# Performance work log

Hardware: AMD Instinct MI355X
Metric: run time of the kernel (lower is better)

The kernel has to match this reference:

```python
import jax, jax.numpy as jnp
import numpy as np

T, B, V, E, NN, ON = 200, 64, 256, 512, 1024, 1024
INIT_P = 3.0


def _lstm_cell(x, h, c, W, b, nn):
    # x: [B, din], h/c: [B, nn], W: [din+nn, 4*nn]
    s = jnp.concatenate([x, h], axis=-1) @ W + b
    sigm_arg, tanh_arg = s[..., : 3 * nn], s[..., 3 * nn :]
    g = jax.nn.sigmoid(sigm_arg)
    f, i, o = g[..., :nn], g[..., nn : 2 * nn], g[..., 2 * nn :]
    c_new = f * c + i * jnp.tanh(tanh_arg)
    h_new = o * jnp.tanh(c_new)
    return h_new, c_new


def setup_inputs() -> dict:
    key = jax.random.key(0)
    ks = jax.random.split(key, 8)

    def n(k, shape, fan_in):
        return jax.random.normal(k, shape, jnp.float32) * jnp.float32(INIT_P * np.sqrt(1.0 / fan_in))

    return {
        "inputs": jax.random.uniform(ks[0], (T, B, V), jnp.float32),
        "h0": jnp.zeros((B, NN), jnp.float32),
        "c0": jnp.zeros((B, NN), jnp.float32),
        "h1": jnp.zeros((B, NN), jnp.float32),
        "c1": jnp.zeros((B, NN), jnp.float32),
        "emb_matrix": n(ks[1], (V, E), V),
        "lstm_w0": n(ks[2], (E + NN, 4 * NN), E + NN),
        "lstm_b0": jnp.zeros((4 * NN,), jnp.float32),
        "lstm_w1": n(ks[3], (NN + NN, 4 * NN), NN + NN),
        "lstm_b1": jnp.zeros((4 * NN,), jnp.float32),
        "out_w0": n(ks[4], (NN, ON), NN),
        "out_b0": jnp.zeros((ON,), jnp.float32),
        "out_w1": n(ks[5], (ON, V), ON),
        "out_b1": jnp.zeros((V,), jnp.float32),
    }


def reference(inputs, h0, c0, h1, c1, emb_matrix, lstm_w0, lstm_b0, lstm_w1,
              lstm_b1, out_w0, out_b0, out_w1, out_b1):
    # embedding: [T,B,V] @ [V,E] -> [T,B,E]
    emb = jnp.einsum("tbv,ve->tbe", inputs, emb_matrix)

    def step(carry, e_t):
        h0_, c0_, h1_, c1_ = carry
        # dropout_keep_prob == 1.0 -> dropout is identity
        h0n, c0n = _lstm_cell(e_t, h0_, c0_, lstm_w0, lstm_b0, NN)
        h1n, c1n = _lstm_cell(h0n, h1_, c1_, lstm_w1, lstm_b1, NN)
        return (h0n, c0n, h1n, c1n), h1n

    _, rnn_outputs = jax.lax.scan(step, (h0, c0, h1, c1), emb)  # [T,B,NN]

    # output module: concat over time (axis 0 for 2-D per-step outputs)
    hs = rnn_outputs.reshape(T * B, NN)
    hs = jax.nn.relu(hs @ out_w0 + out_b0)
    logits = hs @ out_w1 + out_b1  # [T*B, V]
    return logits
```

## Files before the change

### kernel.cpp

```cpp
#include <hip/hip_runtime.h>
#include <hip/hip_bf16.h>
#include <math.h>

#define T_STEPS 200
#define BATCH   64
#define VOCAB   256
#define EMB     512
#define HN      1024
#define ON_     1024
#define SDIM    4096
#define NBLK    256
#define BHN     65536
#define HSLOT   65536
#define ESLOT   32768
#define NGRP    8
#define GSZ     32
#define GTOT    (T_STEPS * 28)
#define W1SPLIT 156

typedef __attribute__((address_space(1))) const void gas_t;
typedef __attribute__((address_space(3))) void las_t;
#define GLDS(gp, lp) __builtin_amdgcn_global_load_lds((gas_t*)(gp), (las_t*)(lp), 16, 0, 0)
#define WAITVM(n) asm volatile("s_waitcnt vmcnt(" #n ")" ::: "memory")
#define LGKM_BAR() do { asm volatile("s_waitcnt lgkmcnt(0)" ::: "memory"); \
    __builtin_amdgcn_s_barrier(); asm volatile("" ::: "memory"); } while (0)

__device__ __forceinline__ float sigmoidf_(float x) {
    return 1.0f / (1.0f + __expf(-x));
}

__device__ __forceinline__ int tidx(int b, int k) {
    return ((k >> 1) << 7) + ((b >> 5) << 6) + (((b & 31) >> 1) << 2) + ((b & 1) << 1) + (k & 1);
}

__device__ __forceinline__ void grid_barrier(int* bar, int step, int bid, int tid, int wv) {
    if (wv < 4) { WAITVM(0); }
    asm volatile("s_waitcnt lgkmcnt(0)" ::: "memory");
    __builtin_amdgcn_s_barrier();
    if (tid == 0) {
        __threadfence();
        const int gidx = bid & (NGRP - 1);
        int* lcnt = bar + gidx * 32;
        int* lgen = bar + (NGRP + gidx) * 32;
        int* gcnt = bar + (2 * NGRP) * 32;
        int* ggen = bar + (2 * NGRP + 1) * 32;
        int a = __hip_atomic_fetch_add(lcnt, 1, __ATOMIC_ACQ_REL, __HIP_MEMORY_SCOPE_AGENT);
        if (a == GSZ * (step + 1) - 1) {
            int b = __hip_atomic_fetch_add(gcnt, 1, __ATOMIC_ACQ_REL, __HIP_MEMORY_SCOPE_AGENT);
            if (b == NGRP * (step + 1) - 1) {
                __hip_atomic_store(ggen, step + 1, __ATOMIC_RELEASE, __HIP_MEMORY_SCOPE_AGENT);
            } else {
                while (__hip_atomic_load(ggen, __ATOMIC_ACQUIRE, __HIP_MEMORY_SCOPE_AGENT) <= step)
                    __builtin_amdgcn_s_sleep(2);
            }
            __hip_atomic_store(lgen, step + 1, __ATOMIC_RELEASE, __HIP_MEMORY_SCOPE_AGENT);
        } else {
            while (__hip_atomic_load(lgen, __ATOMIC_ACQUIRE, __HIP_MEMORY_SCOPE_AGENT) <= step)
                __builtin_amdgcn_s_sleep(2);
        }
        __threadfence();
    }
    asm volatile("" ::: "memory");
    __builtin_amdgcn_s_barrier();
    asm volatile("" ::: "memory");
}

__global__ __launch_bounds__(512, 2)
void lstm_persistent(const float* __restrict__ embT,
                     const float* __restrict__ c0_in, const float* __restrict__ c1_in,
                     const float* __restrict__ Wp0,
                     const float* __restrict__ Wp1a, const float* __restrict__ Wp1b,
                     const float* __restrict__ b0v, const float* __restrict__ b1v,
                     float* __restrict__ h0T, float* __restrict__ HST,
                     const float* __restrict__ h1iT, int* bar)
{
    __shared__ float  Ab[2][8192];
    __shared__ float  Wr[5][2048];
    __shared__ float4 Pred4[8][64][5];
    __shared__ float  Sx[16][66];

    const int tid  = threadIdx.x;
    const int wv   = tid >> 6;
    const int lane = tid & 63;
    const int q    = lane & 15;
    const int c0   = (lane >> 4) << 2;
    const int bid  = blockIdx.x;
    const int colbase = ((bid & 7) << 7) + ((bid >> 3) << 2);

    const float* wp0 = Wp0 + (size_t)bid * ((EMB + HN) * 16);
    const float* wp1 = (bid < W1SPLIT) ? Wp1a + (size_t)bid * (2 * HN * 16)
                                       : Wp1b + (size_t)(bid - W1SPLIT) * (2 * HN * 16);

    float bf0[4], bf1[4], c0r = 0.f, c1r = 0.f;
    if (tid < 256) {
        int gr = tid >> 2, gi = tid & 3;
        c0r = c0_in[gr * HN + colbase + gi];
        c1r = c1_in[gr * HN + colbase + gi];
        #pragma unroll
        for (int gk = 0; gk < 4; ++gk) {
            bf0[gk] = b0v[gk * HN + colbase + gi];
            bf1[gk] = b1v[gk * HN + colbase + gi];
        }
    }

    int g = 0, g5 = 0, buf = 0;

    auto issueW = [&](int gt, int slot) {
        if (gt >= GTOT) return;
        int g28 = gt % 28;
        const float* s = (g28 < 12) ? wp0 + (size_t)g28 * 2048
                                    : wp1 + (size_t)(g28 - 12) * 2048;
        const int j0 = (wv - 4) << 1;
        #pragma unroll
        for (int jj = 0; jj < 2; ++jj) {
            int c = j0 + jj;
            GLDS(s + c * 256 + (lane << 2), &Wr[slot][c << 8]);
        }
    };
    auto issueA = [&](const float* src, int nb) {
        #pragma unroll
        for (int i = 0; i < 8; ++i) {
            int c = (wv << 3) + i;
            GLDS(src + c * 256 + (lane << 2), &Ab[nb][c << 8]);
        }
    };
    auto computeTile = [&](int nb, int wsl, float (&acc)[4][4]) {
        #pragma unroll
        for (int pp = 0; pp < 8; ++pp) {
            const float* ab = &Ab[nb][(((wv << 3) + pp) << 7) + (q << 2)];
            float4 alo = *(const float4*)ab;
            float4 ahi = *(const float4*)(ab + 64);
            const float* wb = &Wr[wsl][(wv << 8) + (pp << 5) + c0];
            float4 w0 = *(const float4*)wb;
            float4 w1 = *(const float4*)(wb + 16);
            acc[0][0]=fmaf(alo.x,w0.x,acc[0][0]); acc[0][1]=fmaf(alo.x,w0.y,acc[0][1]);
            acc[0][2]=fmaf(alo.x,w0.z,acc[0][2]); acc[0][3]=fmaf(alo.x,w0.w,acc[0][3]);
            acc[1][0]=fmaf(alo.z,w0.x,acc[1][0]); acc[1][1]=fmaf(alo.z,w0.y,acc[1][1]);
            acc[1][2]=fmaf(alo.z,w0.z,acc[1][2]); acc[1][3]=fmaf(alo.z,w0.w,acc[1][3]);
            acc[2][0]=fmaf(ahi.x,w0.x,acc[2][0]); acc[2][1]=fmaf(ahi.x,w0.y,acc[2][1]);
            acc[2][2]=fmaf(ahi.x,w0.z,acc[2][2]); acc[2][3]=fmaf(ahi.x,w0.w,acc[2][3]);
            acc[3][0]=fmaf(ahi.z,w0.x,acc[3][0]); acc[3][1]=fmaf(ahi.z,w0.y,acc[3][1]);
            acc[3][2]=fmaf(ahi.z,w0.z,acc[3][2]); acc[3][3]=fmaf(ahi.z,w0.w,acc[3][3]);
            acc[0][0]=fmaf(alo.y,w1.x,acc[0][0]); acc[0][1]=fmaf(alo.y,w1.y,acc[0][1]);
            acc[0][2]=fmaf(alo.y,w1.z,acc[0][2]); acc[0][3]=fmaf(alo.y,w1.w,acc[0][3]);
            acc[1][0]=fmaf(alo.w,w1.x,acc[1][0]); acc[1][1]=fmaf(alo.w,w1.y,acc[1][1]);
            acc[1][2]=fmaf(alo.w,w1.z,acc[1][2]); acc[1][3]=fmaf(alo.w,w1.w,acc[1][3]);
            acc[2][0]=fmaf(ahi.y,w1.x,acc[2][0]); acc[2][1]=fmaf(ahi.y,w1.y,acc[2][1]);
            acc[2][2]=fmaf(ahi.y,w1.z,acc[2][2]); acc[2][3]=fmaf(ahi.y,w1.w,acc[2][3]);
            acc[3][0]=fmaf(ahi.w,w1.x,acc[3][0]); acc[3][1]=fmaf(ahi.w,w1.y,acc[3][1]);
            acc[3][2]=fmaf(ahi.w,w1.z,acc[3][2]); acc[3][3]=fmaf(ahi.w,w1.w,acc[3][3]);
        }
    };
    auto phase = [&](int NT, int split, const float* srcA, const float* srcB,
                     float (&acc)[4][4]) {
        if (wv < 4) { issueA(srcA, buf); WAITVM(0); }
        LGKM_BAR();
        for (int t = 0; t < NT; ++t) {
            if (wv < 4) {
                if (t + 1 < NT) {
                    const float* s = (t + 1 < split) ? srcA + (size_t)(t + 1) * 8192
                                                     : srcB + (size_t)(t + 1 - split) * 8192;
                    issueA(s, buf ^ 1);
                }
            } else {
                int s4 = (g5 + 4 >= 5) ? g5 - 1 : g5 + 4;
                issueW(g + 4, s4);
            }
            computeTile(buf, g5, acc);
            if (wv < 4) {
                if (t + 1 < NT) WAITVM(0);
            } else {
                int rem = GTOT - 1 - g;
                if (rem >= 4)      { WAITVM(6); }
                else if (rem == 3) { WAITVM(4); }
                else if (rem == 2) { WAITVM(2); }
                else if (rem == 1) { WAITVM(0); }
            }
            LGKM_BAR();
            buf ^= 1;
            ++g;
            g5 = (g5 == 4) ? 0 : g5 + 1;
        }
    };
    auto finishCell = [&](float (&acc)[4][4], const float (&bq)[4], float& cr,
                          float* hdst) {
        #pragma unroll
        for (int i = 0; i < 4; ++i)
            Pred4[wv][lane][i] = make_float4(acc[i][0], acc[i][1], acc[i][2], acc[i][3]);
        LGKM_BAR();
        #pragma unroll
        for (int u = 0; u < 2; ++u) {
            int e = (tid << 1) + u;
            int p = e >> 4, ij = e & 15;
            int i = ij >> 2, j = ij & 3;
            float s = 0.f;
            #pragma unroll
            for (int w = 0; w < 8; ++w)
                s += ((const float*)&Pred4[w][p][i])[j];
            int rr = ((i >> 1) << 5) + ((p & 15) << 1) + (i & 1);
            int cl = ((p >> 4) << 2) + j;
            Sx[cl][rr] = s;
        }
        LGKM_BAR();
        if (tid < 256) {
            int gr = tid >> 2, gi = tid & 3;
            float fg = sigmoidf_(Sx[gi][gr]      + bq[0]);
            float ig = sigmoidf_(Sx[4 + gi][gr]  + bq[1]);
            float og = sigmoidf_(Sx[8 + gi][gr]  + bq[2]);
            float gg = tanhf(    Sx[12 + gi][gr] + bq[3]);
            cr = fg * cr + ig * gg;
            hdst[tidx(gr, colbase + gi)] = og * tanhf(cr);
        }
    };

    if (wv >= 4) {
        issueW(0, 0); issueW(1, 1); issueW(2, 2); issueW(3, 3);
        WAITVM(6);
    }

    for (int t = 0; t < T_STEPS; ++t) {
        const float* eT     = embT + (size_t)t * ESLOT;
        const float* h0prev = h0T + (size_t)((t + 1) & 1) * HSLOT;
        float*       h0cur  = h0T + (size_t)(t & 1) * HSLOT;
        const float* h1prev = (t == 0) ? h1iT : HST + (size_t)(t - 1) * HSLOT;
        float*       h1cur  = HST + (size_t)t * HSLOT;

        {
            float acc[4][4] = {};
            phase(12, 4, eT, h0prev, acc);
            finishCell(acc, bf0, c0r, h0cur);
        }
        grid_barrier(bar, t, bid, tid, wv);
        {
            float acc[4][4] = {};
            phase(16, 8, h0cur, h1prev, acc);
            finishCell(acc, bf1, c1r, h1cur);
        }
    }
}

template<int AMODE, int CMODE>
__global__ __launch_bounds__(256)
void gemm128(const float* __restrict__ A, const float* __restrict__ B,
             const float* __restrict__ bias, float* __restrict__ C,
             int M, int N, int K, int relu)
{
    __shared__ float As[16][132];
    __shared__ float Bs[16][64];

    const int tid = threadIdx.x;
    const int tx = tid & 15, ty = tid >> 4;
    const int m0 = blockIdx.y << 7, n0 = blockIdx.x << 6;
    float acc[8][4] = {};

    for (int kk = 0; kk < K; kk += 16) {
        if (AMODE == 0) {
            #pragma unroll
            for (int i = 0; i < 8; ++i) {
                int e = tid + (i << 8);
                int r = e >> 4, k = e & 15;
                As[k][r] = A[(size_t)(m0 + r) * K + kk + k];
            }
        } else if (AMODE == 1) {
            #pragma unroll
            for (int i = 0; i < 8; ++i) {
                int e = tid + (i << 8);
                int k = e >> 7, rr = e & 127;
                int gm = m0 + rr, tt = gm >> 6, b = gm & 63;
                As[k][rr] = A[(size_t)tt * HSLOT + tidx(b, kk + k)];
            }
        } else {
            #pragma unroll
            for (int i = 0; i < 8; ++i) {
                int e = tid + (i << 8);
                int r = e >> 4, k = e & 15;
                As[k][r] = __bfloat162float(
                    ((const __hip_bfloat16*)A)[(size_t)(m0 + r) * K + kk + k]);
            }
        }
        #pragma unroll
        for (int i = 0; i < 4; ++i) {
            int e = tid + (i << 8);
            int r = e >> 6, c = e & 63;
            Bs[r][c] = B[(size_t)(kk + r) * N + n0 + c];
        }
        __syncthreads();
        #pragma unroll
        for (int k = 0; k < 16; ++k) {
            float4 a0 = *(const float4*)&As[k][(ty << 3)];
            float4 a1 = *(const float4*)&As[k][(ty << 3) + 4];
            float4 b4 = *(const float4*)&Bs[k][(tx << 2)];
            float a[8] = {a0.x, a0.y, a0.z, a0.w, a1.x, a1.y, a1.z, a1.w};
            float b[4] = {b4.x, b4.y, b4.z, b4.w};
            #pragma unroll
            for (int i = 0; i < 8; ++i)
                #pragma unroll
                for (int j = 0; j < 4; ++j)
                    acc[i][j] = fmaf(a[i], b[j], acc[i][j]);
        }
        __syncthreads();
    }

    #pragma unroll
    for (int i = 0; i < 8; ++i) {
        int gm = m0 + (ty << 3) + i;
        if (CMODE == 0) {
            float4 o;
            float* op = (float*)&o;
            #pragma unroll
            for (int j = 0; j < 4; ++j) {
                int gn = n0 + (tx << 2) + j;
                float v = acc[i][j] + (bias ? bias[gn] : 0.0f);
                if (relu) v = fmaxf(v, 0.0f);
                op[j] = v;
            }
            *(float4*)&C[(size_t)gm * N + n0 + (tx << 2)] = o;
        } else if (CMODE == 1) {
            int tt = gm >> 6, b = gm & 63;
            int gn = n0 + (tx << 2);
            float* base = C + (size_t)tt * ESLOT;
            *(float2*)&base[tidx(b, gn)]     = make_float2(acc[i][0], acc[i][1]);
            *(float2*)&base[tidx(b, gn + 2)] = make_float2(acc[i][2], acc[i][3]);
        } else {
            #pragma unroll
            for (int j = 0; j < 4; ++j) {
                int gn = n0 + (tx << 2) + j;
                float v = acc[i][j] + (bias ? bias[gn] : 0.0f);
                if (relu) v = fmaxf(v, 0.0f);
                ((__hip_bfloat16*)C)[(size_t)gm * N + gn] = __float2bfloat16(v);
            }
        }
    }
}

__global__ __launch_bounds__(256)
void pack_w(const float* __restrict__ Wsrc, float* __restrict__ WpA,
            float* __restrict__ WpB, int K, int splitB)
{
    long idx = (long)blockIdx.x * 256 + threadIdx.x;
    int c = (int)(idx & 15);
    long r = idx >> 4;
    int b = (int)(r / K);
    int k = (int)(r - (long)b * K);
    int colbase = ((b & 7) << 7) + ((b >> 3) << 2);
    float v = Wsrc[(size_t)k * SDIM + (c >> 2) * HN + colbase + (c & 3)];
    if (b < splitB) WpA[((size_t)b * K + k) * 16 + c] = v;
    else            WpB[((size_t)(b - splitB) * K + k) * 16 + c] = v;
}

__global__ __launch_bounds__(256)
void init_misc(const float* __restrict__ h0_in, const float* __restrict__ h1_in,
               float* __restrict__ h0T, float* __restrict__ h1iT, int* bar)
{
    int i = blockIdx.x * 256 + threadIdx.x;
    if (i < 1024) bar[i] = 0;
    if (i < BHN) {
        int b = i >> 10, col = i & 1023;
        h0T[HSLOT + tidx(b, col)] = h0_in[i];
        h1iT[tidx(b, col)] = h1_in[i];
    }
}

extern "C" void kernel_launch(void* const* d_in, const int* in_sizes, int n_in,
                              void* d_out, int out_size, void* d_ws, size_t ws_size,
                              hipStream_t stream) {
    const float* inputs     = (const float*)d_in[0];
    const float* h0_in      = (const float*)d_in[1];
    const float* c0_in      = (const float*)d_in[2];
    const float* h1_in      = (const float*)d_in[3];
    const float* c1_in      = (const float*)d_in[4];
    const float* emb_matrix = (const float*)d_in[5];
    const float* lstm_w0    = (const float*)d_in[6];
    const float* lstm_b0    = (const float*)d_in[7];
    const float* lstm_w1    = (const float*)d_in[8];
    const float* lstm_b1    = (const float*)d_in[9];
    const float* out_w0     = (const float*)d_in[10];
    const float* out_b0     = (const float*)d_in[11];
    const float* out_w1     = (const float*)d_in[12];
    const float* out_b1     = (const float*)d_in[13];
    float* logits = (float*)d_out;

    const int MB = T_STEPS * BATCH;

    float* ws   = (float*)d_ws;
    float* embT = ws;
    float* Wp0  = embT + (size_t)T_STEPS * ESLOT;
    float* Wp1a = Wp0  + (size_t)NBLK * 1536 * 16;
    float* HST  = Wp1a + (size_t)W1SPLIT * 2048 * 16;
    float* h0T  = HST  + (size_t)T_STEPS * HSLOT;
    float* h1iT = h0T  + 2 * (size_t)HSLOT;
    int*   bar  = (int*)(h1iT + (size_t)BHN);
    __hip_bfloat16* hid = (__hip_bfloat16*)embT;
    float* Wp1b = (float*)d_out;

    init_misc<<<dim3(256), 256, 0, stream>>>(h0_in, h1_in, h0T, h1iT, bar);
    pack_w<<<dim3(24576), 256, 0, stream>>>(lstm_w0, Wp0, Wp0, 1536, NBLK);
    pack_w<<<dim3(32768), 256, 0, stream>>>(lstm_w1, Wp1a, Wp1b, 2048, W1SPLIT);

    gemm128<0, 1><<<dim3(EMB / 64, MB / 128), 256, 0, stream>>>(
        inputs, emb_matrix, nullptr, embT, MB, EMB, VOCAB, 0);

    lstm_persistent<<<dim3(NBLK), 512, 0, stream>>>(
        embT, c0_in, c1_in, Wp0, Wp1a, Wp1b, lstm_b0, lstm_b1,
        h0T, HST, h1iT, bar);

    gemm128<1, 2><<<dim3(ON_ / 64, MB / 128), 256, 0, stream>>>(
        HST, out_w0, out_b0, (float*)hid, MB, ON_, HN, 1);

    gemm128<2, 0><<<dim3(VOCAB / 64, MB / 128), 256, 0, stream>>>(
        (const float*)hid, out_w1, out_b1, logits, MB, VOCAB, ON_, 0);
}
```

Before: 13.07 ms.

## Give each wave private A/W LDS slices with deeper per-wave prefetch, no block barriers

Restructures the LSTM persistent kernel's inner K-loop so every wave loads its own slice of the activation and weight tiles into private LDS buffers. A is triple-buffered and W quadruple-buffered, synchronised only with per-wave vmcnt waits instead of a block-wide barrier per tile. This removes the producer/consumer split between waves 0-3 and 4-7 and the per-tile s_barrier. The partial-sum reduction buffer is halved, at the cost of an extra barrier and an accumulate pass in finishCell. It risks subtle ordering problems in the hand-counted vmcnt values and relies on the grid_barrier and finishCell barriers for cross-phase ordering.

```diff
diff --git a/kernel.cpp b/kernel.cpp
--- a/kernel.cpp
+++ b/kernel.cpp
@@ -22,7 +22,8 @@
 typedef __attribute__((address_space(3))) void las_t;
 #define GLDS(gp, lp) __builtin_amdgcn_global_load_lds((gas_t*)(gp), (las_t*)(lp), 16, 0, 0)
 #define WAITVM(n) asm volatile("s_waitcnt vmcnt(" #n ")" ::: "memory")
-#define LGKM_BAR() do { asm volatile("s_waitcnt lgkmcnt(0)" ::: "memory"); \
+#define LGKM0()   asm volatile("s_waitcnt lgkmcnt(0)" ::: "memory")
+#define LGKM_BAR() do { LGKM0(); \
     __builtin_amdgcn_s_barrier(); asm volatile("" ::: "memory"); } while (0)
 
 __device__ __forceinline__ float sigmoidf_(float x) {
@@ -35,7 +36,7 @@
 
 __device__ __forceinline__ void grid_barrier(int* bar, int step, int bid, int tid, int wv) {
     if (wv < 4) { WAITVM(0); }
-    asm volatile("s_waitcnt lgkmcnt(0)" ::: "memory");
+    LGKM0();
     __builtin_amdgcn_s_barrier();
     if (tid == 0) {
         __threadfence();
@@ -74,9 +75,9 @@
                      float* __restrict__ h0T, float* __restrict__ HST,
                      const float* __restrict__ h1iT, int* bar)
 {
-    __shared__ float  Ab[2][8192];
-    __shared__ float  Wr[5][2048];
-    __shared__ float4 Pred4[8][64][5];
+    __shared__ float  Ab[8][3][1024];
+    __shared__ float  Wr[8][4][256];
+    __shared__ float4 Pred[4][64][5];
     __shared__ float  Sx[16][66];
 
     const int tid  = threadIdx.x;
@@ -87,9 +88,10 @@
     const int bid  = blockIdx.x;
     const int colbase = ((bid & 7) << 7) + ((bid >> 3) << 2);
 
-    const float* wp0 = Wp0 + (size_t)bid * ((EMB + HN) * 16);
-    const float* wp1 = (bid < W1SPLIT) ? Wp1a + (size_t)bid * (2 * HN * 16)
-                                       : Wp1b + (size_t)(bid - W1SPLIT) * (2 * HN * 16);
+    const float* wp0 = Wp0 + (size_t)bid * ((EMB + HN) * 16) + (wv << 8);
+    const float* wp1 = ((bid < W1SPLIT) ? Wp1a + (size_t)bid * (2 * HN * 16)
+                                        : Wp1b + (size_t)(bid - W1SPLIT) * (2 * HN * 16))
+                       + (wv << 8);
 
     float bf0[4], bf1[4], c0r = 0.f, c1r = 0.f;
     if (tid < 256) {
@@ -103,36 +105,30 @@
         }
     }
 
-    int g = 0, g5 = 0, buf = 0;
-
-    auto issueW = [&](int gt, int slot) {
+    int g = 0;
+
+    auto issueW = [&](int gt) {
         if (gt >= GTOT) return;
         int g28 = gt % 28;
         const float* s = (g28 < 12) ? wp0 + (size_t)g28 * 2048
                                     : wp1 + (size_t)(g28 - 12) * 2048;
-        const int j0 = (wv - 4) << 1;
-        #pragma unroll
-        for (int jj = 0; jj < 2; ++jj) {
-            int c = j0 + jj;
-            GLDS(s + c * 256 + (lane << 2), &Wr[slot][c << 8]);
-        }
+        GLDS(s + (lane << 2), &Wr[wv][gt & 3][0]);
     };
-    auto issueA = [&](const float* src, int nb) {
-        #pragma unroll
-        for (int i = 0; i < 8; ++i) {
-            int c = (wv << 3) + i;
-            GLDS(src + c * 256 + (lane << 2), &Ab[nb][c << 8]);
-        }
+    auto issueA = [&](const float* src, int slot) {
+        const float* p = src + (wv << 10) + (lane << 2);
+        #pragma unroll
+        for (int i = 0; i < 4; ++i)
+            GLDS(p + (i << 8), &Ab[wv][slot][i << 8]);
     };
-    auto computeTile = [&](int nb, int wsl, float (&acc)[4][4]) {
+    auto computeTile = [&](int sa, int sw, float (&acc)[4][4]) {
+        const float* abase = &Ab[wv][sa][q << 2];
+        const float* wbase = &Wr[wv][sw][c0];
         #pragma unroll
         for (int pp = 0; pp < 8; ++pp) {
-            const float* ab = &Ab[nb][(((wv << 3) + pp) << 7) + (q << 2)];
-            float4 alo = *(const float4*)ab;
-            float4 ahi = *(const float4*)(ab + 64);
-            const float* wb = &Wr[wsl][(wv << 8) + (pp << 5) + c0];
-            float4 w0 = *(const float4*)wb;
-            float4 w1 = *(const float4*)(wb + 16);
+            float4 alo = *(const float4*)(abase + (pp << 7));
+            float4 ahi = *(const float4*)(abase + (pp << 7) + 64);
+            float4 w0  = *(const float4*)(wbase + (pp << 5));
+            float4 w1  = *(const float4*)(wbase + (pp << 5) + 16);
             acc[0][0]=fmaf(alo.x,w0.x,acc[0][0]); acc[0][1]=fmaf(alo.x,w0.y,acc[0][1]);
             acc[0][2]=fmaf(alo.x,w0.z,acc[0][2]); acc[0][3]=fmaf(alo.x,w0.w,acc[0][3]);
             acc[1][0]=fmaf(alo.z,w0.x,acc[1][0]); acc[1][1]=fmaf(alo.z,w0.y,acc[1][1]);
@@ -151,42 +147,42 @@
             acc[3][2]=fmaf(ahi.w,w1.z,acc[3][2]); acc[3][3]=fmaf(ahi.w,w1.w,acc[3][3]);
         }
     };
-    auto phase = [&](int NT, int split, const float* srcA, const float* srcB,
+    auto phase = [&](int NT, int split, const float* lo, const float* hi,
                      float (&acc)[4][4]) {
-        if (wv < 4) { issueA(srcA, buf); WAITVM(0); }
-        LGKM_BAR();
-        for (int t = 0; t < NT; ++t) {
-            if (wv < 4) {
-                if (t + 1 < NT) {
-                    const float* s = (t + 1 < split) ? srcA + (size_t)(t + 1) * 8192
-                                                     : srcB + (size_t)(t + 1 - split) * 8192;
-                    issueA(s, buf ^ 1);
-                }
-            } else {
-                int s4 = (g5 + 4 >= 5) ? g5 - 1 : g5 + 4;
-                issueW(g + 4, s4);
-            }
-            computeTile(buf, g5, acc);
-            if (wv < 4) {
-                if (t + 1 < NT) WAITVM(0);
-            } else {
-                int rem = GTOT - 1 - g;
-                if (rem >= 4)      { WAITVM(6); }
-                else if (rem == 3) { WAITVM(4); }
-                else if (rem == 2) { WAITVM(2); }
-                else if (rem == 1) { WAITVM(0); }
-            }
-            LGKM_BAR();
-            buf ^= 1;
+        auto srcA = [&](int j) -> const float* {
+            return (j < split) ? lo + (size_t)j * 8192 : hi + (size_t)(j - split) * 8192;
+        };
+        LGKM0();
+        issueA(srcA(0), 0);
+        issueA(srcA(1), 1);
+        for (int j = 0; j < NT; ++j) {
+            LGKM0();
+            issueW(g + 3);
+            if (j + 2 < NT) issueA(srcA(j + 2), (j + 2) % 3);
+            if (j == 0)           { WAITVM(9); }
+            else if (j < NT - 2)  { WAITVM(10); }
+            else if (j == NT - 2) { WAITVM(6); }
+            else                  { WAITVM(2); }
+            computeTile(j % 3, g & 3, acc);
             ++g;
-            g5 = (g5 == 4) ? 0 : g5 + 1;
         }
     };
     auto finishCell = [&](float (&acc)[4][4], const float (&bq)[4], float& cr,
                           float* hdst) {
-        #pragma unroll
-        for (int i = 0; i < 4; ++i)
-            Pred4[wv][lane][i] = make_float4(acc[i][0], acc[i][1], acc[i][2], acc[i][3]);
+        if (wv >= 4) {
+            #pragma unroll
+            for (int i = 0; i < 4; ++i)
+                Pred[wv - 4][lane][i] = make_float4(acc[i][0], acc[i][1], acc[i][2], acc[i][3]);
+        }
+        LGKM_BAR();
+        if (wv < 4) {
+            #pragma unroll
+            for (int i = 0; i < 4; ++i) {
+                float4 p = Pred[wv][lane][i];
+                p.x += acc[i][0]; p.y += acc[i][1]; p.z += acc[i][2]; p.w += acc[i][3];
+                Pred[wv][lane][i] = p;
+            }
+        }
         LGKM_BAR();
         #pragma unroll
         for (int u = 0; u < 2; ++u) {
@@ -195,8 +191,8 @@
             int i = ij >> 2, j = ij & 3;
             float s = 0.f;
             #pragma unroll
-            for (int w = 0; w < 8; ++w)
-                s += ((const float*)&Pred4[w][p][i])[j];
+            for (int w = 0; w < 4; ++w)
+                s += ((const float*)&Pred[w][p][i])[j];
             int rr = ((i >> 1) << 5) + ((p & 15) << 1) + (i & 1);
             int cl = ((p >> 4) << 2) + j;
             Sx[cl][rr] = s;
@@ -213,10 +209,7 @@
         }
     };
 
-    if (wv >= 4) {
-        issueW(0, 0); issueW(1, 1); issueW(2, 2); issueW(3, 3);
-        WAITVM(6);
-    }
+    issueW(0); issueW(1); issueW(2);
 
     for (int t = 0; t < T_STEPS; ++t) {
         const float* eT     = embT + (size_t)t * ESLOT;
```

Result: no change. 12.98 ms (-0.7%).
